# Kernel tuning notes

Measured on AMD Instinct MI355X. Metric: run time of the kernel, lower is better.

Reference implementation:

```python
import jax, jax.numpy as jnp
import numpy as np

EPS = 1e-5
NUM_HEADS = 8


def setup_inputs() -> dict:
    key = jax.random.key(0)
    ks = jax.random.split(key, 4)
    B, C, H, W = 16, 512, 32, 32
    x = jax.random.normal(ks[0], (B, C, H, W), dtype=jnp.float32)
    gn_w = jnp.ones((C,), dtype=jnp.float32)
    gn_b = jnp.zeros((C,), dtype=jnp.float32)
    # 1x1 conv weights stored as [out_ch, in_ch] (kernel dims squeezed)
    qkv_w = jax.random.normal(ks[1], (3 * C, C), dtype=jnp.float32) * (1.0 / np.sqrt(C))
    qkv_b = jnp.zeros((3 * C,), dtype=jnp.float32)
    proj_w = jax.random.normal(ks[2], (C, C), dtype=jnp.float32) * (1.0 / np.sqrt(C))
    proj_b = jnp.zeros((C,), dtype=jnp.float32)
    return {"x": x, "gn_w": gn_w, "gn_b": gn_b, "qkv_w": qkv_w,
            "qkv_b": qkv_b, "proj_w": proj_w, "proj_b": proj_b}


def _group_norm(x, w, b, groups):
    B, C, H, W = x.shape
    xg = x.reshape(B, groups, C // groups, H, W)
    mu = jnp.mean(xg, axis=(2, 3, 4), keepdims=True)
    var = jnp.var(xg, axis=(2, 3, 4), keepdims=True)
    xn = ((xg - mu) * jax.lax.rsqrt(var + EPS)).reshape(B, C, H, W)
    return xn * w[None, :, None, None] + b[None, :, None, None]


def reference(x, gn_w, gn_b, qkv_w, qkv_b, proj_w, proj_b):
    B, C, H, W = x.shape
    heads = NUM_HEADS
    d = C // heads
    residual = x
    xn = _group_norm(x, gn_w, gn_b, heads)
    # 1x1 conv == channel matmul
    qkv = jnp.einsum('oc,bchw->bohw', qkv_w, xn) + qkv_b[None, :, None, None]
    q, k, v = jnp.split(qkv, 3, axis=1)  # each [B, C, H, W]
    q = q.reshape(B, heads, d, H * W)
    k = k.reshape(B, heads, d, H * W)
    v = v.reshape(B, heads, d, H * W)
    scale = 1.0 / np.sqrt(d).astype(np.float32)
    attn = jnp.einsum('bhcn,bhcm->bhnm', q, k) * scale  # [B,h,N,N]
    attn = jax.nn.softmax(attn, axis=-1)
    out = jnp.einsum('bhnm,bhcm->bhcn', attn, v).reshape(B, C, H, W)
    out = jnp.einsum('oc,bchw->bohw', proj_w, out) + proj_b[None, :, None, None]
    return residual + out
```

## Files before the change

### kernel.cpp

```cpp
#include <hip/hip_runtime.h>
#include <hip/hip_bf16.h>
#include <math.h>

typedef short bf16x8 __attribute__((ext_vector_type(8)));
typedef float f32x4  __attribute__((ext_vector_type(4)));
#define MFMA16(a,b,c) __builtin_amdgcn_mfma_f32_16x16x32_bf16(a,b,c,0,0,0)

#define EPSF 1e-5f
#define QSC 0.18033688f

#if __has_builtin(__builtin_amdgcn_exp2f)
#define EXP2(x) __builtin_amdgcn_exp2f(x)
#else
#define EXP2(x) exp2f(x)
#endif

__device__ __forceinline__ unsigned int pk2n(float a, float b){
  __hip_bfloat162 h = __float22bfloat162_rn(make_float2(a, b));
  return *reinterpret_cast<unsigned int*>(&h);
}
__device__ __forceinline__ unsigned short bfn(float f){
  __hip_bfloat16 h = __float2bfloat16(f);
  return *reinterpret_cast<unsigned short*>(&h);
}
__device__ __forceinline__ float4 ld4(const float* p){ return *reinterpret_cast<const float4*>(p); }
__device__ __forceinline__ void st4(float* p, float4 v){ *reinterpret_cast<float4*>(p) = v; }

__device__ __forceinline__ void gl_lds16(const unsigned short* g, unsigned short* l){
  __builtin_amdgcn_global_load_lds(
      (const __attribute__((address_space(1))) unsigned int*)g,
      (__attribute__((address_space(3))) unsigned int*)l, 16, 0, 0);
}

__global__ __launch_bounds__(256,2) void gn_stats_k(const float* __restrict__ x,
                                                    float* __restrict__ stats){
  int blk = blockIdx.x;
  const float4* p4 = reinterpret_cast<const float4*>(x + (size_t)blk * 65536);
  float s1 = 0.f, s2 = 0.f;
  for(int i = threadIdx.x; i < 16384; i += 256){
    float4 v = p4[i];
    s1 += (v.x + v.y) + (v.z + v.w);
    s2 += v.x*v.x + v.y*v.y + v.z*v.z + v.w*v.w;
  }
  #pragma unroll
  for(int off = 32; off; off >>= 1){ s1 += __shfl_xor(s1, off); s2 += __shfl_xor(s2, off); }
  __shared__ float r1[4], r2[4];
  int tid = threadIdx.x;
  if((tid & 63) == 0){ r1[tid >> 6] = s1; r2[tid >> 6] = s2; }
  __syncthreads();
  if(tid == 0){
    float a  = r1[0] + r1[1] + r1[2] + r1[3];
    float b2 = r2[0] + r2[1] + r2[2] + r2[3];
    float mean = a * (1.f / 65536.f);
    float var  = b2 * (1.f / 65536.f) - mean * mean;
    stats[blk]       = mean;
    stats[128 + blk] = rsqrtf(var + EPSF);
  }
}

__global__ __launch_bounds__(256) void wcvt_k(const float* __restrict__ src,
                                              unsigned int* __restrict__ dst){
  int i = blockIdx.x * 256 + threadIdx.x;
  float4 v = reinterpret_cast<const float4*>(src)[i];
  uint2 r; r.x = pk2n(v.x, v.y); r.y = pk2n(v.z, v.w);
  reinterpret_cast<uint2*>(dst)[i] = r;
}

__global__ __launch_bounds__(256) void gnT_k(const float* __restrict__ x,
                                             const float* __restrict__ gnw,
                                             const float* __restrict__ gnb,
                                             const float* __restrict__ stats,
                                             unsigned short* __restrict__ xnT){
  __shared__ float Xl[64 * 65];
  int b = blockIdx.z, c0 = blockIdx.y * 64, n0 = blockIdx.x * 64, tid = threadIdx.x;
  int nq = tid & 15, rr = tid >> 4;
  #pragma unroll
  for(int p = 0; p < 4; p++){
    int cl = p * 16 + rr, c = c0 + cl, gi = c >> 6;
    float mu = stats[b*8 + gi], rs = stats[128 + b*8 + gi];
    float s = rs * gnw[c], t = gnb[c] - mu * s;
    float4 v = *reinterpret_cast<const float4*>(x + ((size_t)(b*512 + c))*1024 + n0 + 4*nq);
    Xl[(4*nq+0)*65 + cl] = v.x*s + t;
    Xl[(4*nq+1)*65 + cl] = v.y*s + t;
    Xl[(4*nq+2)*65 + cl] = v.z*s + t;
    Xl[(4*nq+3)*65 + cl] = v.w*s + t;
  }
  __syncthreads();
  int n = tid >> 2, cq = tid & 3;
  float f[16];
  #pragma unroll
  for(int k = 0; k < 16; k++) f[k] = Xl[n*65 + 16*cq + k];
  uint4 w0, w1;
  w0.x = pk2n(f[0],f[1]);  w0.y = pk2n(f[2],f[3]);  w0.z = pk2n(f[4],f[5]);  w0.w = pk2n(f[6],f[7]);
  w1.x = pk2n(f[8],f[9]);  w1.y = pk2n(f[10],f[11]);w1.z = pk2n(f[12],f[13]);w1.w = pk2n(f[14],f[15]);
  unsigned short* dp = xnT + ((size_t)(b*1024 + n0 + n))*512 + c0 + 16*cq;
  *reinterpret_cast<uint4*>(dp)     = w0;
  *reinterpret_cast<uint4*>(dp + 8) = w1;
}


__global__ __launch_bounds__(256) void qkv_mm(const unsigned short* __restrict__ A,
                                              const unsigned short* __restrict__ Bx,
                                              const float* __restrict__ bias,
                                              unsigned short* __restrict__ T,
                                              unsigned short* __restrict__ V){
  __shared__ __align__(16) unsigned short As[128*64], Bs[128*64];
  int tid = threadIdx.x;
  int n0 = blockIdx.x*128, o0 = blockIdx.y*128, b = blockIdx.z;
  int wid = tid >> 6, wr = wid >> 1, wc = wid & 1, ln = tid & 15, g = (tid >> 4) & 3;
  int l = tid & 63;
  int rsw = (ln & 7) << 3;
  int srow = 32*wid + (l >> 3);
  int scol = (((l & 7) ^ (l >> 3)) << 3);
  const unsigned short* Ag = A  + (size_t)(o0 + srow)*512 + scol;
  const unsigned short* Bg = Bx + ((size_t)(b*1024 + n0 + srow))*512 + scol;
  unsigned short* Asw = As + (32*wid)*64;
  unsigned short* Bsw = Bs + (32*wid)*64;
  f32x4 acc[4][4] = {};
  for(int k0 = 0; k0 < 512; k0 += 64){
    __syncthreads();
    #pragma unroll
    for(int c = 0; c < 4; c++){
      gl_lds16(Ag + (size_t)(8*c)*512 + k0, Asw + (8*c)*64);
      gl_lds16(Bg + (size_t)(8*c)*512 + k0, Bsw + (8*c)*64);
    }
    __syncthreads();
    #pragma unroll
    for(int kh = 0; kh < 2; kh++){
      int ro = (kh*32 + 8*g) ^ rsw;
      bf16x8 af[4], bfv[4];
      #pragma unroll
      for(int mf = 0; mf < 4; mf++)
        af[mf] = *reinterpret_cast<const bf16x8*>(&As[(wr*64 + 16*mf + ln)*64 + ro]);
      #pragma unroll
      for(int nf = 0; nf < 4; nf++)
        bfv[nf] = *reinterpret_cast<const bf16x8*>(&Bs[(wc*64 + 16*nf + ln)*64 + ro]);
      #pragma unroll
      for(int mf = 0; mf < 4; mf++)
        #pragma unroll
        for(int nf = 0; nf < 4; nf++)
          acc[mf][nf] = MFMA16(af[mf], bfv[nf], acc[mf][nf]);
    }
  }
  int obase = o0 + wr*64, nbase = n0 + wc*64;
  __syncthreads();
  unsigned short* scr = (wid < 2 ? As : Bs) + (wid & 1) * 2560;
  float sc = (obase < 512) ? QSC : 1.0f;
  if(obase < 1024){
    #pragma unroll
    for(int h2 = 0; h2 < 2; h2++){
      asm volatile("s_waitcnt lgkmcnt(0)" ::: "memory");
      __builtin_amdgcn_sched_barrier(0);
      #pragma unroll
      for(int mf2 = 0; mf2 < 2; mf2++){
        int mf = 2*h2 + mf2;
        int og = obase + 16*mf + 4*g;
        float b0 = bias[og], b1 = bias[og+1], b2 = bias[og+2], b3 = bias[og+3];
        #pragma unroll
        for(int nf = 0; nf < 4; nf++){
          uint2 pr;
          pr.x = pk2n((acc[mf][nf][0]+b0)*sc, (acc[mf][nf][1]+b1)*sc);
          pr.y = pk2n((acc[mf][nf][2]+b2)*sc, (acc[mf][nf][3]+b3)*sc);
          *reinterpret_cast<uint2*>(&scr[(16*nf + ln)*40 + 16*mf2 + 4*g]) = pr;
        }
      }
      asm volatile("s_waitcnt lgkmcnt(0)" ::: "memory");
      __builtin_amdgcn_sched_barrier(0);
      const unsigned short* rp = &scr[l*40];
      uint4 r0 = *reinterpret_cast<const uint4*>(rp);
      uint4 r1 = *reinterpret_cast<const uint4*>(rp+8);
      uint4 r2 = *reinterpret_cast<const uint4*>(rp+16);
      uint4 r3 = *reinterpret_cast<const uint4*>(rp+24);
      unsigned short* dp = T + ((size_t)(b*1024 + nbase + l))*1024 + obase + 32*h2;
      *reinterpret_cast<uint4*>(dp)    = r0;
      *reinterpret_cast<uint4*>(dp+8)  = r1;
      *reinterpret_cast<uint4*>(dp+16) = r2;
      *reinterpret_cast<uint4*>(dp+24) = r3;
    }
  } else {
    #pragma unroll
    for(int h2 = 0; h2 < 2; h2++){
      asm volatile("s_waitcnt lgkmcnt(0)" ::: "memory");
      __builtin_amdgcn_sched_barrier(0);
      #pragma unroll
      for(int nf2 = 0; nf2 < 2; nf2++){
        int nf = 2*h2 + nf2;
        #pragma unroll
        for(int mf = 0; mf < 4; mf++){
          int og = obase + 16*mf + 4*g;
          #pragma unroll
          for(int r = 0; r < 4; r++)
            scr[(16*mf + 4*g + r)*40 + 16*nf2 + ln] = bfn(acc[mf][nf][r] + bias[og+r]);
        }
      }
      asm volatile("s_waitcnt lgkmcnt(0)" ::: "memory");
      __builtin_amdgcn_sched_barrier(0);
      const unsigned short* rp = &scr[l*40];
      uint4 r0 = *reinterpret_cast<const uint4*>(rp);
      uint4 r1 = *reinterpret_cast<const uint4*>(rp+8);
      uint4 r2 = *reinterpret_cast<const uint4*>(rp+16);
      uint4 r3 = *reinterpret_cast<const uint4*>(rp+24);
      unsigned short* dp = V + ((size_t)(b*512 + obase - 1024 + l))*1024 + nbase + 32*h2;
      *reinterpret_cast<uint4*>(dp)    = r0;
      *reinterpret_cast<uint4*>(dp+8)  = r1;
      *reinterpret_cast<uint4*>(dp+16) = r2;
      *reinterpret_cast<uint4*>(dp+24) = r3;
    }
  }
}

__global__ __launch_bounds__(256) void attn_bf_k(const unsigned short* __restrict__ T,
                                                 const unsigned short* __restrict__ V,
                                                 unsigned short* __restrict__ attT){
  __shared__ __align__(16) unsigned short KT[2][64*64];
  __shared__ __align__(16) unsigned short Vt[2][64*64];
  __shared__ __align__(16) unsigned int   Pl[4*16*32];
  int tid = threadIdx.x;
  int id = blockIdx.x;
  int bh = (id >> 7) * 8 + (id & 7);
  int n0 = ((id >> 3) & 15) * 64;
  int b = bh >> 3, h = bh & 7;
  int wq = tid >> 6, ln = tid & 15, g = (tid >> 4) & 3;
  int l = tid & 63;
  int nl = n0 + wq*16 + ln;
  const unsigned short* Tb = T + ((size_t)b << 20);
  bf16x8 qf0 = *reinterpret_cast<const bf16x8*>(Tb + (size_t)nl*1024 + h*64 + 8*g);
  bf16x8 qf1 = *reinterpret_cast<const bf16x8*>(Tb + (size_t)nl*1024 + h*64 + 32 + 8*g);
  f32x4 acc[4] = {};
  float l_part = 0.f;
  const unsigned short* kg = Tb + 512 + h*64;
  const unsigned short* vg = V + ((size_t)(b*512 + h*64))*1024;
  int pbase = wq*512 + ln*32;
  int psw = (ln & 7) << 2;
  int swz  = (((l & 7) << 3) ^ ((l >> 3) << 3));
  const unsigned short* ksrc = kg + (size_t)(wq*16 + (l>>3))*1024 + swz;
  const unsigned short* vsrc = vg + (size_t)(wq*16 + (l>>3))*1024 + swz;
  int rsw = (ln & 7) << 3;
  int ro0 = (8*g) ^ rsw, ro1 = (32 + 8*g) ^ rsw;
  {
    unsigned short* kb = &KT[0][wq*16*64];
    unsigned short* vb = &Vt[0][wq*16*64];
    gl_lds16(ksrc,            kb);
    gl_lds16(ksrc + 8*1024,   kb + 8*64);
    gl_lds16(vsrc,            vb);
    gl_lds16(vsrc + 8*1024,   vb + 8*64);
  }
  __syncthreads();
  for(int t = 0; t < 16; t++){
    int buf = t & 1;
    if(t < 15){
      int m1 = (t + 1) * 64;
      unsigned short* kb = &KT[buf^1][wq*16*64];
      unsigned short* vb = &Vt[buf^1][wq*16*64];
      gl_lds16(ksrc + (size_t)m1*1024,          kb);
      gl_lds16(ksrc + (size_t)(m1+8)*1024,      kb + 8*64);
      gl_lds16(vsrc + m1,                       vb);
      gl_lds16(vsrc + 8*1024 + m1,              vb + 8*64);
    }
    f32x4 sf[4];
    #pragma unroll
    for(int mf = 0; mf < 4; mf++){
      bf16x8 a0 = *reinterpret_cast<const bf16x8*>(&KT[buf][(16*mf + ln)*64 + ro0]);
      bf16x8 a1 = *reinterpret_cast<const bf16x8*>(&KT[buf][(16*mf + ln)*64 + ro1]);
      f32x4 z = {0.f, 0.f, 0.f, 0.f};
      z = MFMA16(a0, qf0, z);
      sf[mf] = MFMA16(a1, qf1, z);
    }
    float p[16];
    #pragma unroll
    for(int mf = 0; mf < 4; mf++)
      #pragma unroll
      for(int r = 0; r < 4; r++){
        float v = EXP2(sf[mf][r]);
        p[mf*4 + r] = v;
        l_part += v;
      }
    #pragma unroll
    for(int mt = 0; mt < 4; mt++){
      Pl[pbase + ((8*mt + 2*g + 0) ^ psw)] = pk2n(p[4*mt + 0], p[4*mt + 1]);
      Pl[pbase + ((8*mt + 2*g + 1) ^ psw)] = pk2n(p[4*mt + 2], p[4*mt + 3]);
    }
    asm volatile("s_waitcnt lgkmcnt(0)" ::: "memory");
    __builtin_amdgcn_sched_barrier(0);
    union { uint4 u; bf16x8 hv; } pb0, pb1;
    pb0.u = *reinterpret_cast<const uint4*>(&Pl[pbase + ((4*g) ^ psw)]);
    pb1.u = *reinterpret_cast<const uint4*>(&Pl[pbase + ((16 + 4*g) ^ psw)]);
    #pragma unroll
    for(int cf = 0; cf < 4; cf++){
      bf16x8 v0 = *reinterpret_cast<const bf16x8*>(&Vt[buf][(16*cf + ln)*64 + ro0]);
      bf16x8 v1 = *reinterpret_cast<const bf16x8*>(&Vt[buf][(16*cf + ln)*64 + ro1]);
      acc[cf] = MFMA16(v0, pb0.hv, acc[cf]);
      acc[cf] = MFMA16(v1, pb1.hv, acc[cf]);
    }
    __syncthreads();
  }
  float lsum = l_part;
  lsum += __shfl_xor(lsum, 16);
  lsum += __shfl_xor(lsum, 32);
  float inv = 1.f / lsum;
  unsigned short* op = attT + ((size_t)(b*1024 + nl))*512 + h*64;
  #pragma unroll
  for(int cf = 0; cf < 4; cf++){
    uint2 pr;
    pr.x = pk2n(acc[cf][0]*inv, acc[cf][1]*inv);
    pr.y = pk2n(acc[cf][2]*inv, acc[cf][3]*inv);
    *reinterpret_cast<uint2*>(op + 16*cf + 4*g) = pr;
  }
}

__global__ __launch_bounds__(256) void proj_mm(const unsigned short* __restrict__ A,
                                               const unsigned short* __restrict__ Bx,
                                               const float* __restrict__ bias,
                                               const float* __restrict__ resid,
                                               float* __restrict__ out){
  __shared__ __align__(16) unsigned short As[128*64], Bs[128*64];
  int tid = threadIdx.x;
  int n0 = blockIdx.x*128, o0 = blockIdx.y*128, b = blockIdx.z;
  int wid = tid >> 6, wr = wid >> 1, wc = wid & 1, ln = tid & 15, g = (tid >> 4) & 3;
  int l = tid & 63;
  int rsw = (ln & 7) << 3;
  int srow = 32*wid + (l >> 3);
  int scol = (((l & 7) ^ (l >> 3)) << 3);
  const unsigned short* Ag = A  + (size_t)(o0 + srow)*512 + scol;
  const unsigned short* Bg = Bx + ((size_t)(b*1024 + n0 + srow))*512 + scol;
  unsigned short* Asw = As + (32*wid)*64;
  unsigned short* Bsw = Bs + (32*wid)*64;
  f32x4 acc[4][4] = {};
  for(int k0 = 0; k0 < 512; k0 += 64){
    __syncthreads();
    #pragma unroll
    for(int c = 0; c < 4; c++){
      gl_lds16(Ag + (size_t)(8*c)*512 + k0, Asw + (8*c)*64);
      gl_lds16(Bg + (size_t)(8*c)*512 + k0, Bsw + (8*c)*64);
    }
    __syncthreads();
    #pragma unroll
    for(int kh = 0; kh < 2; kh++){
      int ro = (kh*32 + 8*g) ^ rsw;
      bf16x8 af[4], bfv[4];
      #pragma unroll
      for(int mf = 0; mf < 4; mf++)
        af[mf] = *reinterpret_cast<const bf16x8*>(&As[(wr*64 + 16*mf + ln)*64 + ro]);
      #pragma unroll
      for(int nf = 0; nf < 4; nf++)
        bfv[nf] = *reinterpret_cast<const bf16x8*>(&Bs[(wc*64 + 16*nf + ln)*64 + ro]);
      #pragma unroll
      for(int mf = 0; mf < 4; mf++)
        #pragma unroll
        for(int nf = 0; nf < 4; nf++)
          acc[mf][nf] = MFMA16(af[mf], bfv[nf], acc[mf][nf]);
    }
  }
  #pragma unroll
  for(int mf = 0; mf < 4; mf++)
    #pragma unroll
    for(int r = 0; r < 4; r++){
      int o = o0 + wr*64 + 16*mf + 4*g + r;
      float bo = bias[o];
      #pragma unroll
      for(int nf = 0; nf < 4; nf++){
        int n = n0 + wc*64 + 16*nf + ln;
        size_t off = ((size_t)(b*512 + o))*1024 + n;
        out[off] = acc[mf][nf][r] + bo + resid[off];
      }
    }
}

extern "C" void kernel_launch(void* const* d_in, const int* in_sizes, int n_in,
                              void* d_out, int out_size, void* d_ws, size_t ws_size,
                              hipStream_t stream){
  const float* x     = (const float*)d_in[0];
  const float* gnw   = (const float*)d_in[1];
  const float* gnb   = (const float*)d_in[2];
  const float* qkvw  = (const float*)d_in[3];
  const float* qkvb  = (const float*)d_in[4];
  const float* projw = (const float*)d_in[5];
  const float* projb = (const float*)d_in[6];
  float* out = (float*)d_out;

  char* w = (char*)d_ws;
  float* stats = (float*)w;            w += 1024;
  unsigned short* wqb = (unsigned short*)w;  w += (size_t)1536*512*2;
  unsigned short* wpb = (unsigned short*)w;  w += (size_t)512*512*2;
  unsigned short* xnT = (unsigned short*)w;  w += (size_t)16*1024*512*2;
  unsigned short* Tqk = (unsigned short*)w;  w += (size_t)16*1024*1024*2;
  unsigned short* Vb  = (unsigned short*)w;  w += (size_t)16*512*1024*2;
  unsigned short* attT = (unsigned short*)w; w += (size_t)16*1024*512*2;

  hipLaunchKernelGGL(gn_stats_k, dim3(128), dim3(256), 0, stream, x, stats);
  hipLaunchKernelGGL(wcvt_k, dim3(768), dim3(256), 0, stream, qkvw, (unsigned int*)wqb);
  hipLaunchKernelGGL(wcvt_k, dim3(256), dim3(256), 0, stream, projw, (unsigned int*)wpb);
  hipLaunchKernelGGL(gnT_k, dim3(16, 8, 16), dim3(256), 0, stream, x, gnw, gnb, stats, xnT);
  hipLaunchKernelGGL(qkv_mm, dim3(8, 12, 16), dim3(256), 0, stream, wqb, xnT, qkvb, Tqk, Vb);
  hipLaunchKernelGGL(attn_bf_k, dim3(2048), dim3(256), 0, stream, Tqk, Vb, attT);
  hipLaunchKernelGGL(proj_mm, dim3(8, 4, 16), dim3(256), 0, stream, wpb, attT, projb, x, out);
}
```

Before: 161.1 us.

## Fuse GroupNorm stats into transpose kernel and feed P to MFMA from registers

Merges the GroupNorm statistics kernel and the normalize-transpose kernel into one kernel per (batch, group) that computes mean and rstd and then writes the bf16 transposed tile. This removes a launch and the stats round trip, but the grid shrinks to 128 blocks. In attention, when the 16x16x16 bf16 MFMA builtin exists, the softmax probabilities go straight from registers as the B operand instead of passing through LDS. This removes the Pl shared-memory round trip and its waitcnt, at the cost of twice as many smaller MFMAs and a changed V read pattern.

New measurement: 160.1 us. No clear change (-0.6%).

```diff
diff --git a/kernel.cpp b/kernel.cpp
--- a/kernel.cpp
+++ b/kernel.cpp
@@ -3,8 +3,16 @@
 #include <math.h>
 
 typedef short bf16x8 __attribute__((ext_vector_type(8)));
+typedef short bf16x4 __attribute__((ext_vector_type(4)));
 typedef float f32x4  __attribute__((ext_vector_type(4)));
 #define MFMA16(a,b,c) __builtin_amdgcn_mfma_f32_16x16x32_bf16(a,b,c,0,0,0)
+
+#if __has_builtin(__builtin_amdgcn_mfma_f32_16x16x16bf16_1k)
+#define HAVE_MFMA16X16 1
+#define MFMAK16(a,b,c) __builtin_amdgcn_mfma_f32_16x16x16bf16_1k(a,b,c,0,0,0)
+#else
+#define HAVE_MFMA16X16 0
+#endif
 
 #define EPSF 1e-5f
 #define QSC 0.18033688f
@@ -30,32 +38,6 @@
   __builtin_amdgcn_global_load_lds(
       (const __attribute__((address_space(1))) unsigned int*)g,
       (__attribute__((address_space(3))) unsigned int*)l, 16, 0, 0);
-}
-
-__global__ __launch_bounds__(256,2) void gn_stats_k(const float* __restrict__ x,
-                                                    float* __restrict__ stats){
-  int blk = blockIdx.x;
-  const float4* p4 = reinterpret_cast<const float4*>(x + (size_t)blk * 65536);
-  float s1 = 0.f, s2 = 0.f;
-  for(int i = threadIdx.x; i < 16384; i += 256){
-    float4 v = p4[i];
-    s1 += (v.x + v.y) + (v.z + v.w);
-    s2 += v.x*v.x + v.y*v.y + v.z*v.z + v.w*v.w;
-  }
-  #pragma unroll
-  for(int off = 32; off; off >>= 1){ s1 += __shfl_xor(s1, off); s2 += __shfl_xor(s2, off); }
-  __shared__ float r1[4], r2[4];
-  int tid = threadIdx.x;
-  if((tid & 63) == 0){ r1[tid >> 6] = s1; r2[tid >> 6] = s2; }
-  __syncthreads();
-  if(tid == 0){
-    float a  = r1[0] + r1[1] + r1[2] + r1[3];
-    float b2 = r2[0] + r2[1] + r2[2] + r2[3];
-    float mean = a * (1.f / 65536.f);
-    float var  = b2 * (1.f / 65536.f) - mean * mean;
-    stats[blk]       = mean;
-    stats[128 + blk] = rsqrtf(var + EPSF);
-  }
 }
 
 __global__ __launch_bounds__(256) void wcvt_k(const float* __restrict__ src,
@@ -66,36 +48,59 @@
   reinterpret_cast<uint2*>(dst)[i] = r;
 }
 
-__global__ __launch_bounds__(256) void gnT_k(const float* __restrict__ x,
-                                             const float* __restrict__ gnw,
-                                             const float* __restrict__ gnb,
-                                             const float* __restrict__ stats,
-                                             unsigned short* __restrict__ xnT){
-  __shared__ float Xl[64 * 65];
-  int b = blockIdx.z, c0 = blockIdx.y * 64, n0 = blockIdx.x * 64, tid = threadIdx.x;
-  int nq = tid & 15, rr = tid >> 4;
+__global__ __launch_bounds__(512) void gn_fused_k(const float* __restrict__ x,
+                                                  const float* __restrict__ gnw,
+                                                  const float* __restrict__ gnb,
+                                                  unsigned short* __restrict__ xnT){
+  __shared__ float Xl[2][64*65];
+  __shared__ float red[16];
+  int blk = blockIdx.x;
+  int b = blk >> 3, g = blk & 7;
+  int tid = threadIdx.x;
+  const float4* p4 = reinterpret_cast<const float4*>(x + (size_t)blk * 65536);
+  float s1 = 0.f, s2 = 0.f;
+  for(int i = tid; i < 16384; i += 512){
+    float4 v = p4[i];
+    s1 += (v.x + v.y) + (v.z + v.w);
+    s2 += v.x*v.x + v.y*v.y + v.z*v.z + v.w*v.w;
+  }
   #pragma unroll
-  for(int p = 0; p < 4; p++){
-    int cl = p * 16 + rr, c = c0 + cl, gi = c >> 6;
-    float mu = stats[b*8 + gi], rs = stats[128 + b*8 + gi];
-    float s = rs * gnw[c], t = gnb[c] - mu * s;
-    float4 v = *reinterpret_cast<const float4*>(x + ((size_t)(b*512 + c))*1024 + n0 + 4*nq);
-    Xl[(4*nq+0)*65 + cl] = v.x*s + t;
-    Xl[(4*nq+1)*65 + cl] = v.y*s + t;
-    Xl[(4*nq+2)*65 + cl] = v.z*s + t;
-    Xl[(4*nq+3)*65 + cl] = v.w*s + t;
-  }
+  for(int off = 32; off; off >>= 1){ s1 += __shfl_xor(s1, off); s2 += __shfl_xor(s2, off); }
+  if((tid & 63) == 0){ red[tid >> 6] = s1; red[8 + (tid >> 6)] = s2; }
   __syncthreads();
-  int n = tid >> 2, cq = tid & 3;
-  float f[16];
+  float a = 0.f, b2 = 0.f;
   #pragma unroll
-  for(int k = 0; k < 16; k++) f[k] = Xl[n*65 + 16*cq + k];
-  uint4 w0, w1;
-  w0.x = pk2n(f[0],f[1]);  w0.y = pk2n(f[2],f[3]);  w0.z = pk2n(f[4],f[5]);  w0.w = pk2n(f[6],f[7]);
-  w1.x = pk2n(f[8],f[9]);  w1.y = pk2n(f[10],f[11]);w1.z = pk2n(f[12],f[13]);w1.w = pk2n(f[14],f[15]);
-  unsigned short* dp = xnT + ((size_t)(b*1024 + n0 + n))*512 + c0 + 16*cq;
-  *reinterpret_cast<uint4*>(dp)     = w0;
-  *reinterpret_cast<uint4*>(dp + 8) = w1;
+  for(int w = 0; w < 8; w++){ a += red[w]; b2 += red[8 + w]; }
+  float mean = a * (1.f / 65536.f);
+  float rstd = rsqrtf(b2 * (1.f / 65536.f) - mean * mean + EPSF);
+  int half = tid >> 8, t256 = tid & 255;
+  int nq = t256 & 15, rr = t256 >> 4;
+  int c0 = g * 64;
+  for(int it = 0; it < 8; it++){
+    int n0 = (it*2 + half) * 64;
+    __syncthreads();
+    #pragma unroll
+    for(int p = 0; p < 4; p++){
+      int cl = p * 16 + rr, c = c0 + cl;
+      float s = rstd * gnw[c], t = gnb[c] - mean * s;
+      float4 v = ld4(x + ((size_t)(b*512 + c))*1024 + n0 + 4*nq);
+      Xl[half][(4*nq+0)*65 + cl] = v.x*s + t;
+      Xl[half][(4*nq+1)*65 + cl] = v.y*s + t;
+      Xl[half][(4*nq+2)*65 + cl] = v.z*s + t;
+      Xl[half][(4*nq+3)*65 + cl] = v.w*s + t;
+    }
+    __syncthreads();
+    int n = t256 >> 2, cq = t256 & 3;
+    float f[16];
+    #pragma unroll
+    for(int k = 0; k < 16; k++) f[k] = Xl[half][n*65 + 16*cq + k];
+    uint4 w0, w1;
+    w0.x = pk2n(f[0],f[1]);  w0.y = pk2n(f[2],f[3]);  w0.z = pk2n(f[4],f[5]);  w0.w = pk2n(f[6],f[7]);
+    w1.x = pk2n(f[8],f[9]);  w1.y = pk2n(f[10],f[11]);w1.z = pk2n(f[12],f[13]);w1.w = pk2n(f[14],f[15]);
+    unsigned short* dp = xnT + ((size_t)(b*1024 + n0 + n))*512 + c0 + 16*cq;
+    *reinterpret_cast<uint4*>(dp)     = w0;
+    *reinterpret_cast<uint4*>(dp + 8) = w1;
+  }
 }
 
 
@@ -214,7 +219,9 @@
                                                  unsigned short* __restrict__ attT){
   __shared__ __align__(16) unsigned short KT[2][64*64];
   __shared__ __align__(16) unsigned short Vt[2][64*64];
+#if !HAVE_MFMA16X16
   __shared__ __align__(16) unsigned int   Pl[4*16*32];
+#endif
   int tid = threadIdx.x;
   int id = blockIdx.x;
   int bh = (id >> 7) * 8 + (id & 7);
@@ -230,13 +237,20 @@
   float l_part = 0.f;
   const unsigned short* kg = Tb + 512 + h*64;
   const unsigned short* vg = V + ((size_t)(b*512 + h*64))*1024;
-  int pbase = wq*512 + ln*32;
-  int psw = (ln & 7) << 2;
   int swz  = (((l & 7) << 3) ^ ((l >> 3) << 3));
   const unsigned short* ksrc = kg + (size_t)(wq*16 + (l>>3))*1024 + swz;
   const unsigned short* vsrc = vg + (size_t)(wq*16 + (l>>3))*1024 + swz;
   int rsw = (ln & 7) << 3;
   int ro0 = (8*g) ^ rsw, ro1 = (32 + 8*g) ^ rsw;
+#if HAVE_MFMA16X16
+  int vcol[4];
+  #pragma unroll
+  for(int mf = 0; mf < 4; mf++)
+    vcol[mf] = (((2*mf + (g>>1)) ^ (ln & 7)) << 3) + 4*(g & 1);
+#else
+  int pbase = wq*512 + ln*32;
+  int psw = (ln & 7) << 2;
+#endif
   {
     unsigned short* kb = &KT[0][wq*16*64];
     unsigned short* vb = &Vt[0][wq*16*64];
@@ -275,6 +289,24 @@
         p[mf*4 + r] = v;
         l_part += v;
       }
+#if HAVE_MFMA16X16
+    bf16x4 pb[4];
+    #pragma unroll
+    for(int mf = 0; mf < 4; mf++){
+      union { uint2 u; bf16x4 h; } cv;
+      cv.u.x = pk2n(p[4*mf + 0], p[4*mf + 1]);
+      cv.u.y = pk2n(p[4*mf + 2], p[4*mf + 3]);
+      pb[mf] = cv.h;
+    }
+    #pragma unroll
+    for(int cf = 0; cf < 4; cf++){
+      #pragma unroll
+      for(int mf = 0; mf < 4; mf++){
+        bf16x4 va = *reinterpret_cast<const bf16x4*>(&Vt[buf][(16*cf + ln)*64 + vcol[mf]]);
+        acc[cf] = MFMAK16(va, pb[mf], acc[cf]);
+      }
+    }
+#else
     #pragma unroll
     for(int mt = 0; mt < 4; mt++){
       Pl[pbase + ((8*mt + 2*g + 0) ^ psw)] = pk2n(p[4*mt + 0], p[4*mt + 1]);
@@ -292,6 +324,7 @@
       acc[cf] = MFMA16(v0, pb0.hv, acc[cf]);
       acc[cf] = MFMA16(v1, pb1.hv, acc[cf]);
     }
+#endif
     __syncthreads();
   }
   float lsum = l_part;
@@ -379,7 +412,6 @@
   float* out = (float*)d_out;
 
   char* w = (char*)d_ws;
-  float* stats = (float*)w;            w += 1024;
   unsigned short* wqb = (unsigned short*)w;  w += (size_t)1536*512*2;
   unsigned short* wpb = (unsigned short*)w;  w += (size_t)512*512*2;
   unsigned short* xnT = (unsigned short*)w;  w += (size_t)16*1024*512*2;
@@ -387,10 +419,9 @@
   unsigned short* Vb  = (unsigned short*)w;  w += (size_t)16*512*1024*2;
   unsigned short* attT = (unsigned short*)w; w += (size_t)16*1024*512*2;
 
-  hipLaunchKernelGGL(gn_stats_k, dim3(128), dim3(256), 0, stream, x, stats);
   hipLaunchKernelGGL(wcvt_k, dim3(768), dim3(256), 0, stream, qkvw, (unsigned int*)wqb);
   hipLaunchKernelGGL(wcvt_k, dim3(256), dim3(256), 0, stream, projw, (unsigned int*)wpb);
-  hipLaunchKernelGGL(gnT_k, dim3(16, 8, 16), dim3(256), 0, stream, x, gnw, gnb, stats, xnT);
+  hipLaunchKernelGGL(gn_fused_k, dim3(128), dim3(512), 0, stream, x, gnw, gnb, xnT);
   hipLaunchKernelGGL(qkv_mm, dim3(8, 12, 16), dim3(256), 0, stream, wqb, xnT, qkvb, Tqk, Vb);
   hipLaunchKernelGGL(attn_bf_k, dim3(2048), dim3(256), 0, stream, Tqk, Vb, attT);
   hipLaunchKernelGGL(proj_mm, dim3(8, 4, 16), dim3(256), 0, stream, wpb, attT, projb, x, out);
```
